# Optimization experiments

Hardware: AMD Instinct MI355X
Metric: run time of the kernel (lower is better)

## Reference

```python
import jax, jax.numpy as jnp
import numpy as np

N, T, F, H = 16384, 16, 256, 16
DH = F // H
SAMPLE_MASKS = [0, 1, 3, 4, 7, 9, 12, 14, 17, 19, 23, 26, 28, 31, 35, 38]
NEG_BIG = float(-2**32 + 1)


def setup_inputs() -> dict:
    key = jax.random.key(0)
    ks = jax.random.split(key, 7)
    sc = 0.05  # keep pre-softmax logits in a sane range
    return {
        "x": jax.random.normal(ks[0], (N, T, F), jnp.float32),
        "pos_emb": jax.random.normal(ks[1], (T, F), jnp.float32) * sc,
        "Wq": jax.random.normal(ks[2], (F, F), jnp.float32) * sc,
        "Wk": jax.random.normal(ks[3], (F, F), jnp.float32) * sc,
        "Wv": jax.random.normal(ks[4], (F, F), jnp.float32) * sc,
        "lin_w": jax.random.normal(ks[5], (F, F), jnp.float32) * sc,
        "lin_b": jnp.zeros((F,), jnp.float32),
    }


def reference(x, pos_emb, Wq, Wk, Wv, lin_w, lin_b):
    # temporal decay mask (method == 1): entry (i,j) = t_i - t_j for i>j, else 1
    sm = jnp.asarray(SAMPLE_MASKS[:T], jnp.float32)
    idx = jnp.arange(T)
    lower = idx[:, None] > idx[None, :]            # strictly lower triangle
    time_info = jnp.where(lower, sm[:, None] - sm[None, :], 1.0)  # [T,T]
    causal = idx[:, None] >= idx[None, :]          # tril incl. diagonal

    temporal = x + pos_emb[None, :, :]             # [N,T,F]
    # QKV projections and head split (contiguous feature chunks per head)
    q = jnp.einsum('ntf,fe->nte', temporal, Wq).reshape(N, T, H, DH)
    k = jnp.einsum('ntf,fe->nte', temporal, Wk).reshape(N, T, H, DH)
    v = jnp.einsum('ntf,fe->nte', temporal, Wv).reshape(N, T, H, DH)

    scores = jnp.einsum('nihd,njhd->nhij', q, k) / jnp.float32(T) ** 0.5
    scores = scores / time_info                    # divisive temporal decay
    scores = jnp.where(causal, scores, jnp.float32(NEG_BIG))
    attn = jax.nn.softmax(scores, axis=-1)         # [N,H,T,T]

    out = jnp.einsum('nhij,njhd->nihd', attn, v).reshape(N, T, F)
    # feedforward: relu(Linear(out)) + out
    out = jax.nn.relu(out @ lin_w.T + lin_b) + out
    # residual with position-augmented inputs
    return out + temporal
```

## Files before the change

kernel.cpp:

```cpp
#include <hip/hip_runtime.h>

using short8  = __attribute__((ext_vector_type(8))) short;
using f32x4   = __attribute__((ext_vector_type(4))) float;

namespace {
constexpr int T_  = 16;
constexpr int F_  = 256;
constexpr int LDA = 260;
constexpr int QLD = 772;

__device__ __forceinline__ unsigned short f32_to_bf16_rn(float v) {
  unsigned u = __builtin_bit_cast(unsigned, v);
  unsigned r = u + 0x7FFFu + ((u >> 16) & 1u);
  return (unsigned short)(r >> 16);
}
__device__ __forceinline__ void split_hi_lo(float v, unsigned short& h, unsigned short& l) {
  unsigned u = __builtin_bit_cast(unsigned, v);
  unsigned r = (u + 0x7FFFu + ((u >> 16) & 1u)) & 0xFFFF0000u;
  h = (unsigned short)(r >> 16);
  float lo = v - __builtin_bit_cast(float, r);
  l = f32_to_bf16_rn(lo);
}
}

extern "C" __global__ void __launch_bounds__(256)
build_frags(const float* __restrict__ Wq, const float* __restrict__ Wk,
            const float* __restrict__ Wv, const float* __restrict__ linw,
            unsigned short* __restrict__ frag) {
  const int g = blockIdx.x * 256 + threadIdx.x;
  const int l = g & 63;
  const int chunk = g >> 6;
  const int s = chunk & 7;
  const int tile = chunk >> 3;
  const int lr = l & 15, lg = l >> 4;
  const int kbase = s * 32 + lg * 8;
  unsigned short v[8];
  if (tile < 48) {
    const int n = tile * 16 + lr;
    const float* src = (n < 256) ? (Wq + n) : ((n < 512) ? (Wk + (n - 256)) : (Wv + (n - 512)));
#pragma unroll
    for (int j = 0; j < 8; ++j) v[j] = f32_to_bf16_rn(src[(kbase + j) * F_]);
  } else {
    const int e = (tile - 48) * 16 + lr;
    const float* src = linw + e * F_ + kbase;
#pragma unroll
    for (int j = 0; j < 8; ++j) v[j] = f32_to_bf16_rn(src[j]);
  }
  short8 pack;
#pragma unroll
  for (int j = 0; j < 8; ++j) pack[j] = (short)v[j];
  *(short8*)(frag + chunk * 512 + l * 8) = pack;
}

extern "C" __global__ void __launch_bounds__(256, 2)
fused_temporal_attn(const float* __restrict__ x, const float* __restrict__ pos_emb,
                    const unsigned short* __restrict__ frag,
                    const float* __restrict__ lin_b, float* __restrict__ out) {
  __shared__ float sTemp[T_][LDA];
  __shared__ float sQKV[T_][QLD];

  const int n = blockIdx.x;
  const int tid = threadIdx.x;

  {
    const float4* x4 = (const float4*)(x + (size_t)n * (T_ * F_));
    const float4* p4 = (const float4*)pos_emb;
#pragma unroll
    for (int it = 0; it < 4; ++it) {
      const int f4 = tid + it * 256;
      float4 a = x4[f4];
      const float4 b = p4[f4];
      a.x += b.x; a.y += b.y; a.z += b.z; a.w += b.w;
      const int row = f4 >> 6, c4 = f4 & 63;
      *(float4*)&sTemp[row][c4 * 4] = a;
    }
  }
  __syncthreads();

  const int wv = tid >> 6;
  const int l  = tid & 63;
  const int lr = l & 15;
  const int lg = l >> 4;

  {
    f32x4 acc[12];
#pragma unroll
    for (int t = 0; t < 12; ++t) acc[t] = (f32x4){0.f, 0.f, 0.f, 0.f};

#pragma unroll 2
    for (int s = 0; s < 8; ++s) {
      const float* ap = &sTemp[lr][s * 32 + lg * 8];
      const float4 a0 = *(const float4*)ap;
      const float4 a1 = *(const float4*)(ap + 4);
      const float av[8] = {a0.x, a0.y, a0.z, a0.w, a1.x, a1.y, a1.z, a1.w};
      short8 ah, al;
#pragma unroll
      for (int j = 0; j < 8; ++j) {
        unsigned short hh, ll;
        split_hi_lo(av[j], hh, ll);
        ah[j] = (short)hh; al[j] = (short)ll;
      }
      const unsigned short* bp = frag + (size_t)((wv * 12) * 8 + s) * 512 + l * 8;
#pragma unroll
      for (int t = 0; t < 12; ++t) {
        const short8 b = *(const short8*)(bp + t * 4096);
        acc[t] = __builtin_amdgcn_mfma_f32_16x16x32_bf16(ah, b, acc[t], 0, 0, 0);
        acc[t] = __builtin_amdgcn_mfma_f32_16x16x32_bf16(al, b, acc[t], 0, 0, 0);
      }
    }
#pragma unroll
    for (int t = 0; t < 12; ++t) {
      const int col = (wv * 12 + t) * 16 + lr;
#pragma unroll
      for (int r = 0; r < 4; ++r) sQKV[lg * 4 + r][col] = acc[t][r];
    }
  }
  __syncthreads();

  {
    const int h = tid >> 4;
    const int i = tid & 15;
    constexpr float SMV[16] = {0.f, 1.f, 3.f, 4.f, 7.f, 9.f, 12.f, 14.f,
                               17.f, 19.f, 23.f, 26.f, 28.f, 31.f, 35.f, 38.f};
    const float smi = SMV[i];

    float qv[16];
#pragma unroll
    for (int dd = 0; dd < 4; ++dd) {
      const float4 q4 = *(const float4*)&sQKV[i][h * 16 + dd * 4];
      qv[4 * dd + 0] = q4.x; qv[4 * dd + 1] = q4.y; qv[4 * dd + 2] = q4.z; qv[4 * dd + 3] = q4.w;
    }

    float p[16];
    float mx = -3.0e38f;
#pragma unroll
    for (int j = 0; j < 16; ++j) {
      float dot = 0.f;
#pragma unroll
      for (int dd = 0; dd < 4; ++dd) {
        const float4 k4 = *(const float4*)&sQKV[j][F_ + h * 16 + dd * 4];
        dot = fmaf(qv[4 * dd + 0], k4.x, dot);
        dot = fmaf(qv[4 * dd + 1], k4.y, dot);
        dot = fmaf(qv[4 * dd + 2], k4.z, dot);
        dot = fmaf(qv[4 * dd + 3], k4.w, dot);
      }
      const float diff = (j < i) ? (smi - SMV[j]) : 1.0f;
      float sc = (dot * 0.25f) / diff;
      sc = (j <= i) ? sc : -3.0e38f;
      p[j] = sc;
      mx = fmaxf(mx, sc);
    }
    float den = 0.f;
#pragma unroll
    for (int j = 0; j < 16; ++j) {
      float e = __expf(p[j] - mx);
      e = (j <= i) ? e : 0.f;
      p[j] = e;
      den += e;
    }
    const float inv = 1.0f / den;

    float o[16];
#pragma unroll
    for (int d = 0; d < 16; ++d) o[d] = 0.f;
#pragma unroll
    for (int j = 0; j < 16; ++j) {
      const float pj = p[j] * inv;
#pragma unroll
      for (int dd = 0; dd < 4; ++dd) {
        const float4 v4 = *(const float4*)&sQKV[j][2 * F_ + h * 16 + dd * 4];
        o[4 * dd + 0] = fmaf(pj, v4.x, o[4 * dd + 0]);
        o[4 * dd + 1] = fmaf(pj, v4.y, o[4 * dd + 1]);
        o[4 * dd + 2] = fmaf(pj, v4.z, o[4 * dd + 2]);
        o[4 * dd + 3] = fmaf(pj, v4.w, o[4 * dd + 3]);
      }
    }
    __syncthreads();
#pragma unroll
    for (int dd = 0; dd < 4; ++dd)
      *(float4*)&sQKV[i][h * 16 + dd * 4] =
          make_float4(o[4 * dd + 0], o[4 * dd + 1], o[4 * dd + 2], o[4 * dd + 3]);
  }
  __syncthreads();

  {
    f32x4 fa[4];
#pragma unroll
    for (int t = 0; t < 4; ++t) fa[t] = (f32x4){0.f, 0.f, 0.f, 0.f};

#pragma unroll 2
    for (int s = 0; s < 8; ++s) {
      const float* ap = &sQKV[lr][s * 32 + lg * 8];
      const float4 a0 = *(const float4*)ap;
      const float4 a1 = *(const float4*)(ap + 4);
      const float av[8] = {a0.x, a0.y, a0.z, a0.w, a1.x, a1.y, a1.z, a1.w};
      short8 ah, al;
#pragma unroll
      for (int j = 0; j < 8; ++j) {
        unsigned short hh, ll;
        split_hi_lo(av[j], hh, ll);
        ah[j] = (short)hh; al[j] = (short)ll;
      }
      const unsigned short* bp = frag + (size_t)((48 + wv * 4) * 8 + s) * 512 + l * 8;
#pragma unroll
      for (int t = 0; t < 4; ++t) {
        const short8 b = *(const short8*)(bp + t * 4096);
        fa[t] = __builtin_amdgcn_mfma_f32_16x16x32_bf16(ah, b, fa[t], 0, 0, 0);
        fa[t] = __builtin_amdgcn_mfma_f32_16x16x32_bf16(al, b, fa[t], 0, 0, 0);
      }
    }

    float* outp = out + (size_t)n * (T_ * F_);
#pragma unroll
    for (int t = 0; t < 4; ++t) {
      const int col = (wv * 4 + t) * 16 + lr;
      const float bias = lin_b[col];
#pragma unroll
      for (int r = 0; r < 4; ++r) {
        const int row = lg * 4 + r;
        const float val = fmaxf(fa[t][r] + bias, 0.f) + sQKV[row][col] + sTemp[row][col];
        outp[row * F_ + col] = val;
      }
    }
  }
}

extern "C" void kernel_launch(void* const* d_in, const int* in_sizes, int n_in,
                              void* d_out, int out_size, void* d_ws, size_t ws_size,
                              hipStream_t stream) {
  const float* x   = (const float*)d_in[0];
  const float* pos = (const float*)d_in[1];
  const float* Wq  = (const float*)d_in[2];
  const float* Wk  = (const float*)d_in[3];
  const float* Wv  = (const float*)d_in[4];
  const float* lw  = (const float*)d_in[5];
  const float* lb  = (const float*)d_in[6];
  float* out = (float*)d_out;
  unsigned short* frag = (unsigned short*)d_ws;

  build_frags<<<128, 256, 0, stream>>>(Wq, Wk, Wv, lw, frag);
  fused_temporal_attn<<<16384, 256, 0, stream>>>(x, pos, frag, lb, out);
}
```

Before: 788.9 us.

## Drop temporal LDS buffer, pre-split A fragments in registers, raise occupancy

Removes the separate sTemp shared buffer and stages x+pos_emb through the sQKV buffer in MFMA fragment order. Each lane then converts its A fragments to bf16 hi/lo once for all 8 k-steps and keeps them in registers, which cuts repeated LDS reads and split work inside the QKV loop. The smaller LDS footprint allows the launch bound to rise to 3 blocks per CU. In exchange, the final residual re-reads x and pos_emb from global memory, and the 16 short8 fragments add register pressure that the tighter launch bound may turn into spills.

```diff
diff --git a/kernel.cpp b/kernel.cpp
--- a/kernel.cpp
+++ b/kernel.cpp
@@ -6,7 +6,6 @@
 namespace {
 constexpr int T_  = 16;
 constexpr int F_  = 256;
-constexpr int LDA = 260;
 constexpr int QLD = 772;
 
 __device__ __forceinline__ unsigned short f32_to_bf16_rn(float v) {
@@ -52,60 +51,62 @@
   *(short8*)(frag + chunk * 512 + l * 8) = pack;
 }
 
-extern "C" __global__ void __launch_bounds__(256, 2)
+extern "C" __global__ void __launch_bounds__(256, 3)
 fused_temporal_attn(const float* __restrict__ x, const float* __restrict__ pos_emb,
                     const unsigned short* __restrict__ frag,
                     const float* __restrict__ lin_b, float* __restrict__ out) {
-  __shared__ float sTemp[T_][LDA];
   __shared__ float sQKV[T_][QLD];
 
   const int n = blockIdx.x;
   const int tid = threadIdx.x;
-
-  {
-    const float4* x4 = (const float4*)(x + (size_t)n * (T_ * F_));
-    const float4* p4 = (const float4*)pos_emb;
-#pragma unroll
-    for (int it = 0; it < 4; ++it) {
-      const int f4 = tid + it * 256;
-      float4 a = x4[f4];
-      const float4 b = p4[f4];
-      a.x += b.x; a.y += b.y; a.z += b.z; a.w += b.w;
-      const int row = f4 >> 6, c4 = f4 & 63;
-      *(float4*)&sTemp[row][c4 * 4] = a;
-    }
-  }
-  __syncthreads();
-
   const int wv = tid >> 6;
   const int l  = tid & 63;
   const int lr = l & 15;
   const int lg = l >> 4;
 
+  const float* __restrict__ xb = x + (size_t)n * (T_ * F_);
+
+  {
+#pragma unroll
+    for (int it = 0; it < 4; ++it) {
+      const int sh = it * 4 + wv;
+      const int k0 = (sh >> 1) * 32 + lg * 8 + (sh & 1) * 4;
+      float4 a = *(const float4*)(xb + lr * 256 + k0);
+      const float4 b = *(const float4*)(pos_emb + lr * 256 + k0);
+      a.x += b.x; a.y += b.y; a.z += b.z; a.w += b.w;
+      *(float4*)&sQKV[sh][l * 4] = a;
+    }
+  }
+  __syncthreads();
+
+  short8 ah[8], al[8];
+#pragma unroll
+  for (int s = 0; s < 8; ++s) {
+    const float4 a0 = *(const float4*)&sQKV[2 * s][l * 4];
+    const float4 a1 = *(const float4*)&sQKV[2 * s + 1][l * 4];
+    const float av[8] = {a0.x, a0.y, a0.z, a0.w, a1.x, a1.y, a1.z, a1.w};
+#pragma unroll
+    for (int j = 0; j < 8; ++j) {
+      unsigned short hh, ll;
+      split_hi_lo(av[j], hh, ll);
+      ah[s][j] = (short)hh; al[s][j] = (short)ll;
+    }
+  }
+  __syncthreads();
+
   {
     f32x4 acc[12];
 #pragma unroll
     for (int t = 0; t < 12; ++t) acc[t] = (f32x4){0.f, 0.f, 0.f, 0.f};
 
-#pragma unroll 2
+#pragma unroll
     for (int s = 0; s < 8; ++s) {
-      const float* ap = &sTemp[lr][s * 32 + lg * 8];
-      const float4 a0 = *(const float4*)ap;
-      const float4 a1 = *(const float4*)(ap + 4);
-      const float av[8] = {a0.x, a0.y, a0.z, a0.w, a1.x, a1.y, a1.z, a1.w};
-      short8 ah, al;
-#pragma unroll
-      for (int j = 0; j < 8; ++j) {
-        unsigned short hh, ll;
-        split_hi_lo(av[j], hh, ll);
-        ah[j] = (short)hh; al[j] = (short)ll;
-      }
       const unsigned short* bp = frag + (size_t)((wv * 12) * 8 + s) * 512 + l * 8;
 #pragma unroll
       for (int t = 0; t < 12; ++t) {
         const short8 b = *(const short8*)(bp + t * 4096);
-        acc[t] = __builtin_amdgcn_mfma_f32_16x16x32_bf16(ah, b, acc[t], 0, 0, 0);
-        acc[t] = __builtin_amdgcn_mfma_f32_16x16x32_bf16(al, b, acc[t], 0, 0, 0);
+        acc[t] = __builtin_amdgcn_mfma_f32_16x16x32_bf16(ah[s], b, acc[t], 0, 0, 0);
+        acc[t] = __builtin_amdgcn_mfma_f32_16x16x32_bf16(al[s], b, acc[t], 0, 0, 0);
       }
     }
 #pragma unroll
@@ -194,19 +195,19 @@
       const float4 a0 = *(const float4*)ap;
       const float4 a1 = *(const float4*)(ap + 4);
       const float av[8] = {a0.x, a0.y, a0.z, a0.w, a1.x, a1.y, a1.z, a1.w};
-      short8 ah, al;
+      short8 fh, fl;
 #pragma unroll
       for (int j = 0; j < 8; ++j) {
         unsigned short hh, ll;
         split_hi_lo(av[j], hh, ll);
-        ah[j] = (short)hh; al[j] = (short)ll;
+        fh[j] = (short)hh; fl[j] = (short)ll;
       }
       const unsigned short* bp = frag + (size_t)((48 + wv * 4) * 8 + s) * 512 + l * 8;
 #pragma unroll
       for (int t = 0; t < 4; ++t) {
         const short8 b = *(const short8*)(bp + t * 4096);
-        fa[t] = __builtin_amdgcn_mfma_f32_16x16x32_bf16(ah, b, fa[t], 0, 0, 0);
-        fa[t] = __builtin_amdgcn_mfma_f32_16x16x32_bf16(al, b, fa[t], 0, 0, 0);
+        fa[t] = __builtin_amdgcn_mfma_f32_16x16x32_bf16(fh, b, fa[t], 0, 0, 0);
+        fa[t] = __builtin_amdgcn_mfma_f32_16x16x32_bf16(fl, b, fa[t], 0, 0, 0);
       }
     }
 
@@ -218,7 +219,8 @@
 #pragma unroll
       for (int r = 0; r < 4; ++r) {
         const int row = lg * 4 + r;
-        const float val = fmaxf(fa[t][r] + bias, 0.f) + sQKV[row][col] + sTemp[row][col];
+        const float temporal = xb[row * 256 + col] + pos_emb[row * 256 + col];
+        const float val = fmaxf(fa[t][r] + bias, 0.f) + sQKV[row][col] + temporal;
         outp[row * F_ + col] = val;
       }
     }
```

Result: slower. 904.4 us (+14.6%).
